# Optimization experiments

Hardware: AMD Instinct MI355X
Metric: run time of the kernel (lower is better)

Reference implementation:

```python
import jax, jax.numpy as jnp
import numpy as np

N1 = 50000; N2 = 50000; E1 = 800000; E2 = 800000; A = 10000
D_IN = 128; NHID = 128; D_OUT = 128; RATIO = 0.5
N_SUP = int(N1 * RATIO)  # 25000 super nodes
K_HOPS = 10  # GCN(in, nhid, k=10)
NEG_INF = jnp.float32(-1e30)


def _edge_norm(src, dst, w, n):
    # symmetric degree normalization of edge weights
    deg = jax.ops.segment_sum(w, dst, num_segments=n) + 1.0
    return w * jax.lax.rsqrt(deg[src] * deg[dst])


def _prop(h, src, dst, norm, n):
    # one round of weighted message passing: h'[v] = sum_e norm_e * h[src_e]
    return jax.ops.segment_sum(norm[:, None] * h[src], dst, num_segments=n)


def _gcn_k(x, src, dst, norm, n, W, b):
    h = x @ W + b
    for _ in range(K_HOPS):
        h = _prop(h, src, dst, norm, n)
    return h


def setup_inputs() -> dict:
    key = jax.random.key(0)
    ks = jax.random.split(key, 24)
    s = 0.05
    return {
        "x": jax.random.normal(ks[0], (N1, D_IN), jnp.float32),
        "edge_index": jax.random.randint(ks[1], (2, E1), 0, N1, jnp.int32),
        "edge_weight": jax.random.uniform(ks[2], (E1,), jnp.float32),
        "y": jax.random.normal(ks[3], (N2, D_IN), jnp.float32),
        "edge_index_y": jax.random.randint(ks[4], (2, E2), 0, N2, jnp.int32),
        "edge_weight_y": jax.random.uniform(ks[5], (E2,), jnp.float32),
        "anchor_links": jax.random.randint(ks[6], (2, A), 0, N1, jnp.int32),
        "temperature": 1,
        "W_gcn": jax.random.normal(ks[7], (D_IN, NHID), jnp.float32) * s,
        "b_gcn": jnp.zeros((NHID,), jnp.float32),
        "p_score": jax.random.normal(ks[8], (NHID,), jnp.float32) * s,
        "W_conv1": jax.random.normal(ks[9], (NHID, NHID), jnp.float32) * s,
        "b_conv1": jnp.zeros((NHID,), jnp.float32),
        "W_mlp1": jax.random.normal(ks[10], (NHID, NHID), jnp.float32) * s,
        "b_mlp1": jnp.zeros((NHID,), jnp.float32),
        "W_l1": jax.random.normal(ks[11], (NHID, NHID), jnp.float32) * s,
        "W_l2": jax.random.normal(ks[12], (NHID, NHID), jnp.float32) * s,
        "W_mlp2": jax.random.normal(ks[13], (NHID, D_OUT), jnp.float32) * s,
        "b_mlp2": jnp.zeros((D_OUT,), jnp.float32),
    }


def reference(x, edge_index, edge_weight, y, edge_index_y, edge_weight_y,
              anchor_links, temperature, W_gcn, b_gcn, p_score, W_conv1,
              b_conv1, W_mlp1, b_mlp1, W_l1, W_l2, W_mlp2, b_mlp2):
    T = jnp.float32(temperature)
    src, dst = edge_index[0], edge_index[1]
    norm1 = _edge_norm(src, dst, edge_weight, N1)

    # ---- down_convs[0]: 10-hop GCN on graph 1 ----
    out_x = _gcn_k(x, src, dst, norm1, N1, W_gcn, b_gcn)  # xs[0]
    xr = jax.nn.relu(out_x)

    # ---- TransPool: score -> top-k super nodes -> attention assignment ----
    s = xr @ p_score                             # [N1]
    _, perm = jax.lax.top_k(s, N_SUP)            # original ids of super nodes
    sup_id = jnp.full((N1,), -1, jnp.int32).at[perm].set(
        jnp.arange(N_SUP, dtype=jnp.int32))
    self_ids = jnp.arange(N1, dtype=src.dtype)
    cand_node = jnp.concatenate([src, self_ids])  # node being assigned
    cand_sup = jnp.concatenate([dst, self_ids])   # candidate super node
    valid = sup_id[cand_sup] >= 0
    att = jnp.sum(xr[cand_node] * xr[cand_sup], axis=-1)
    att = att / (jnp.sqrt(jnp.float32(NHID)) * T)
    att = jnp.where(valid, att, NEG_INF)
    m = jax.ops.segment_max(att, cand_node, num_segments=N1)
    e = jnp.exp(att - m[cand_node])
    esum = jax.ops.segment_sum(e, cand_node, num_segments=N1)
    w_soft = e / esum[cand_node]                 # per-node softmax over candidates
    is_best = valid & (att >= m[cand_node])
    cluster = jnp.full((N1,), -1, jnp.int32).at[cand_node].max(
        jnp.where(is_best, sup_id[cand_sup], -1))
    has = cluster >= 0
    cluster = jnp.maximum(cluster, 0)
    match = is_best & (sup_id[cand_sup] == cluster[cand_node])
    a = jnp.zeros((N1,), jnp.float32).at[cand_node].max(
        jnp.where(match, w_soft, 0.0))
    a = jnp.where(has, a, 0.0)                   # assign_weight (P1 values)

    # coarsen: x' = P x ; A' = P A P^T via cluster relabeling
    x_pool = jax.ops.segment_sum(a[:, None] * xr, cluster, num_segments=N_SUP)
    csrc, cdst = cluster[src], cluster[dst]
    cw = edge_weight * a[src] * a[dst]

    # ---- down_convs[1]: GCNConv on coarse graph (with self loop) ----
    norm_c = _edge_norm(csrc, cdst, cw, N_SUP)
    h2 = x_pool @ W_conv1 + b_conv1
    h2 = _prop(h2, csrc, cdst, norm_c, N_SUP) + h2
    sup1 = jax.nn.relu(h2)                       # xs[1]

    # ---- MLP1 ----
    sup2 = jax.nn.relu(sup1 @ W_mlp1 + b_mlp1)

    # ---- Q = P1 @ L (sparse-sparse matmul) ----
    a1, a2 = anchor_links[0], anchor_links[1]
    anchor_w = jnp.ones((A,), jnp.float32)
    q_sup = cluster[a1]
    q_col = a2
    q_w = a[a1] * anchor_w

    # ---- graph 2: shared down_convs[0] ----
    srcy, dsty = edge_index_y[0], edge_index_y[1]
    normy = _edge_norm(srcy, dsty, edge_weight_y, N2)
    out_y = _gcn_k(y, srcy, dsty, normy, N2, W_gcn, b_gcn)

    # ---- LastLayer: Q^T (sup2 W_l1) + L^T (out_x W_l2) scattered into graph2 ----
    t1 = sup2 @ W_l1
    out_y = out_y + jax.ops.segment_sum(q_w[:, None] * t1[q_sup], q_col,
                                        num_segments=N2)
    t2 = out_x @ W_l2
    out_y = out_y + jax.ops.segment_sum(anchor_w[:, None] * t2[a1], a2,
                                        num_segments=N2)

    recon_y = out_y @ W_mlp2 + b_mlp2
    return (out_x, sup1, out_y, sup2, a, recon_y)
```

## Files before the change

kernel.cpp:

```cpp
#include <hip/hip_runtime.h>
#include <hip/hip_bf16.h>
#include <math.h>

#define N1 50000
#define N2 50000
#define E1C 800000
#define E2C 800000
#define AC 10000
#define F 128
#define NSUP 25000
#define KHOPS 10
#define NEGINF -1e30f
#define NBINS 65536
#define NBINS22 (1 << 22)

static inline int cdiv(int a, int b) { return (a + b - 1) / b; }

__device__ __forceinline__ float bf2f(unsigned short u) {
  return __uint_as_float(((unsigned)u) << 16);
}
__device__ __forceinline__ unsigned short f2bf(float f) {
  unsigned x = __float_as_uint(f);
  return (unsigned short)((x + 0x7FFFu + ((x >> 16) & 1u)) >> 16);
}

__global__ void k_count(const int* __restrict__ key, int* __restrict__ cnt, int n) {
  int e = blockIdx.x * blockDim.x + threadIdx.x;
  if (e < n) atomicAdd(&cnt[key[e]], 1);
}

__global__ void k_scan(const int* __restrict__ cnt, int* __restrict__ rowptr, int n) {
  const int T = 1024;
  int t = threadIdx.x;
  int vpt = (n + T - 1) / T;
  int lo = t * vpt, hi = lo + vpt;
  if (hi > n) hi = n;
  int sum = 0;
  for (int i = lo; i < hi; ++i) sum += cnt[i];
  int lane = t & 63, wid = t >> 6;
  int v = sum;
#pragma unroll
  for (int o = 1; o < 64; o <<= 1) {
    int u = __shfl_up(v, o, 64);
    if (lane >= o) v += u;
  }
  __shared__ int wsum[16];
  if (lane == 63) wsum[wid] = v;
  __syncthreads();
  if (t < 16) {
    int w = wsum[t];
#pragma unroll
    for (int o = 1; o < 16; o <<= 1) {
      int u = __shfl_up(w, o, 64);
      if (t >= o) w += u;
    }
    wsum[t] = w;
  }
  __syncthreads();
  int base = (wid ? wsum[wid - 1] : 0) + (v - sum);
  if (t == 0) rowptr[0] = 0;
  int run = base;
  for (int i = lo; i < hi; ++i) { run += cnt[i]; rowptr[i + 1] = run; }
}

__global__ void k_fill(const int* __restrict__ key, const int* __restrict__ payload,
                       const float* __restrict__ val, const int* __restrict__ rowptr,
                       int* __restrict__ cnt, int* __restrict__ col, float* __restrict__ v,
                       int n) {
  int e = blockIdx.x * blockDim.x + threadIdx.x;
  if (e < n) {
    int k = key[e];
    int p = atomicAdd(&cnt[k], 1);
    int s = rowptr[k] + p;
    col[s] = payload[e];
    if (val) v[s] = val[e];
  }
}

__global__ void k_fill_iota(const int* __restrict__ key, const int* __restrict__ rowptr,
                            int* __restrict__ cnt, int* __restrict__ col, int n) {
  int e = blockIdx.x * blockDim.x + threadIdx.x;
  if (e < n) {
    int k = key[e];
    int p = atomicAdd(&cnt[k], 1);
    col[rowptr[k] + p] = e;
  }
}

__global__ void k_count_coarse(const int* __restrict__ dst, const int* __restrict__ cluster,
                               int* __restrict__ cnt, int n) {
  int e = blockIdx.x * blockDim.x + threadIdx.x;
  if (e < n) atomicAdd(&cnt[cluster[dst[e]]], 1);
}

__global__ void k_fill_coarse(const int* __restrict__ src, const int* __restrict__ dst,
                              const int* __restrict__ cluster, const float* __restrict__ w,
                              const float* __restrict__ a, const int* __restrict__ rowptr,
                              int* __restrict__ cnt, int* __restrict__ col,
                              float* __restrict__ v, int n) {
  int e = blockIdx.x * blockDim.x + threadIdx.x;
  if (e < n) {
    int sd = dst[e];
    int k = cluster[sd];
    int p = atomicAdd(&cnt[k], 1);
    int s = rowptr[k] + p;
    int ss = src[e];
    col[s] = cluster[ss];
    v[s] = w[e] * a[ss] * a[sd];
  }
}

__global__ void k_rowsum(const int* __restrict__ rowptr, const float* __restrict__ v,
                         float* __restrict__ deg, int n) {
  int row = blockIdx.x * 8 + (threadIdx.x >> 5);
  if (row >= n) return;
  int q = threadIdx.x & 31;
  int s0 = rowptr[row], s1 = rowptr[row + 1];
  float s = 0.f;
  for (int k = s0 + q; k < s1; k += 32) s += v[k];
#pragma unroll
  for (int o = 16; o; o >>= 1) s += __shfl_xor(s, o, 64);
  if (q == 0) deg[row] = s;
}

__global__ void k_csrnorm(const int* __restrict__ rowptr, const int* __restrict__ col,
                          float* __restrict__ v, const float* __restrict__ deg, int n) {
  int row = blockIdx.x * 8 + (threadIdx.x >> 5);
  if (row >= n) return;
  int q = threadIdx.x & 31;
  int s0 = rowptr[row], s1 = rowptr[row + 1];
  float di = deg[row] + 1.f;
  for (int s = s0 + q; s < s1; s += 32) {
    float dc = deg[col[s]] + 1.f;
    v[s] = v[s] / sqrtf(dc * di);
  }
}

__global__ void k_prop(const float4* __restrict__ hin, float4* __restrict__ hout,
                       float4* __restrict__ relu_out, const int* __restrict__ rowptr,
                       const int* __restrict__ col, const float* __restrict__ val, int n) {
  int node = blockIdx.x * 8 + (threadIdx.x >> 5);
  if (node >= n) return;
  int q = threadIdx.x & 31;
  int s0 = rowptr[node], s1 = rowptr[node + 1];
  float4 acc = make_float4(0.f, 0.f, 0.f, 0.f);
  for (int s = s0; s < s1; s += 8) {
    int c[8]; float v[8];
#pragma unroll
    for (int j = 0; j < 8; ++j) {
      int ss = s + j;
      int sc = (ss < s1) ? ss : (s1 - 1);
      c[j] = col[sc];
      v[j] = (ss < s1) ? val[sc] : 0.f;
    }
    float4 h[8];
#pragma unroll
    for (int j = 0; j < 8; ++j) h[j] = hin[(size_t)c[j] * 32 + q];
#pragma unroll
    for (int j = 0; j < 8; ++j) {
      acc.x = fmaf(v[j], h[j].x, acc.x);
      acc.y = fmaf(v[j], h[j].y, acc.y);
      acc.z = fmaf(v[j], h[j].z, acc.z);
      acc.w = fmaf(v[j], h[j].w, acc.w);
    }
  }
  hout[(size_t)node * 32 + q] = acc;
  if (relu_out) {
    float4 r;
    r.x = fmaxf(acc.x, 0.f); r.y = fmaxf(acc.y, 0.f);
    r.z = fmaxf(acc.z, 0.f); r.w = fmaxf(acc.w, 0.f);
    relu_out[(size_t)node * 32 + q] = r;
  }
}

__global__ void k_prop_bf16(const ushort4* __restrict__ hin, ushort4* __restrict__ hout,
                            float4* __restrict__ fout, const int* __restrict__ rowptr,
                            const int* __restrict__ col, const float* __restrict__ val, int n) {
  int node = blockIdx.x * 8 + (threadIdx.x >> 5);
  if (node >= n) return;
  int q = threadIdx.x & 31;
  int s0 = rowptr[node], s1 = rowptr[node + 1];
  float4 acc = make_float4(0.f, 0.f, 0.f, 0.f);
  for (int s = s0; s < s1; s += 8) {
    int c[8]; float v[8];
#pragma unroll
    for (int j = 0; j < 8; ++j) {
      int ss = s + j;
      int sc = (ss < s1) ? ss : (s1 - 1);
      c[j] = col[sc];
      v[j] = (ss < s1) ? val[sc] : 0.f;
    }
    ushort4 h[8];
#pragma unroll
    for (int j = 0; j < 8; ++j) h[j] = hin[(size_t)c[j] * 32 + q];
#pragma unroll
    for (int j = 0; j < 8; ++j) {
      acc.x = fmaf(v[j], bf2f(h[j].x), acc.x);
      acc.y = fmaf(v[j], bf2f(h[j].y), acc.y);
      acc.z = fmaf(v[j], bf2f(h[j].z), acc.z);
      acc.w = fmaf(v[j], bf2f(h[j].w), acc.w);
    }
  }
  if (fout) {
    fout[(size_t)node * 32 + q] = acc;
  } else {
    ushort4 o;
    o.x = f2bf(acc.x); o.y = f2bf(acc.y); o.z = f2bf(acc.z); o.w = f2bf(acc.w);
    hout[(size_t)node * 32 + q] = o;
  }
}

__global__ void k_transpose(const float* __restrict__ W, float* __restrict__ WT) {
  int i = blockIdx.x * blockDim.x + threadIdx.x;
  if (i < F * F) { int k = i >> 7, c = i & 127; WT[c * F + k] = W[i]; }
}

__global__ void k_mm128(const float* __restrict__ X, const float* __restrict__ WT,
                        const float* __restrict__ bias, float* __restrict__ out,
                        int M, int relu) {
  __shared__ float4 xs[16][32];
  int tid = threadIdx.x;
  int c = tid & 127;
  int half = tid >> 7;
  int row0 = blockIdx.x * 16;
  for (int t = tid; t < 512; t += 256) {
    int r = t >> 5, k4 = t & 31;
    int gr = row0 + r;
    float4 v = make_float4(0.f, 0.f, 0.f, 0.f);
    if (gr < M) v = ((const float4*)X)[(size_t)gr * 32 + k4];
    xs[r][k4] = v;
  }
  __syncthreads();
  float acc[8];
#pragma unroll
  for (int r = 0; r < 8; ++r) acc[r] = 0.f;
  const float4* wrow = (const float4*)WT + (size_t)c * 32;
  for (int k4 = 0; k4 < 32; ++k4) {
    float4 w = wrow[k4];
#pragma unroll
    for (int r = 0; r < 8; ++r) {
      float4 xv = xs[half * 8 + r][k4];
      acc[r] = fmaf(xv.x, w.x, acc[r]);
      acc[r] = fmaf(xv.y, w.y, acc[r]);
      acc[r] = fmaf(xv.z, w.z, acc[r]);
      acc[r] = fmaf(xv.w, w.w, acc[r]);
    }
  }
  float bb = bias ? bias[c] : 0.f;
#pragma unroll
  for (int r = 0; r < 8; ++r) {
    int gr = row0 + half * 8 + r;
    if (gr < M) {
      float v = acc[r] + bb;
      if (relu) v = fmaxf(v, 0.f);
      out[(size_t)gr * F + c] = v;
    }
  }
}

__global__ void k_mm128_bf16(const float* __restrict__ X, const float* __restrict__ WT,
                             const float* __restrict__ bias, unsigned short* __restrict__ out,
                             int M) {
  __shared__ float4 xs[16][32];
  int tid = threadIdx.x;
  int c = tid & 127;
  int half = tid >> 7;
  int row0 = blockIdx.x * 16;
  for (int t = tid; t < 512; t += 256) {
    int r = t >> 5, k4 = t & 31;
    int gr = row0 + r;
    float4 v = make_float4(0.f, 0.f, 0.f, 0.f);
    if (gr < M) v = ((const float4*)X)[(size_t)gr * 32 + k4];
    xs[r][k4] = v;
  }
  __syncthreads();
  float acc[8];
#pragma unroll
  for (int r = 0; r < 8; ++r) acc[r] = 0.f;
  const float4* wrow = (const float4*)WT + (size_t)c * 32;
  for (int k4 = 0; k4 < 32; ++k4) {
    float4 w = wrow[k4];
#pragma unroll
    for (int r = 0; r < 8; ++r) {
      float4 xv = xs[half * 8 + r][k4];
      acc[r] = fmaf(xv.x, w.x, acc[r]);
      acc[r] = fmaf(xv.y, w.y, acc[r]);
      acc[r] = fmaf(xv.z, w.z, acc[r]);
      acc[r] = fmaf(xv.w, w.w, acc[r]);
    }
  }
  float bb = bias ? bias[c] : 0.f;
#pragma unroll
  for (int r = 0; r < 8; ++r) {
    int gr = row0 + half * 8 + r;
    if (gr < M) out[(size_t)gr * F + c] = f2bf(acc[r] + bb);
  }
}

__global__ void k_addrelu(const float* __restrict__ a, const float* __restrict__ b,
                          float* __restrict__ out, int n) {
  int i = blockIdx.x * blockDim.x + threadIdx.x;
  if (i < n) out[i] = fmaxf(a[i] + b[i], 0.f);
}

__global__ void k_score(const float* __restrict__ xr, const float* __restrict__ p,
                        float* __restrict__ s, int n) {
  int wid = (blockIdx.x * blockDim.x + threadIdx.x) >> 6;
  int lane = threadIdx.x & 63;
  if (wid >= n) return;
  const float* row = xr + (size_t)wid * F;
  float d = row[lane] * p[lane] + row[lane + 64] * p[lane + 64];
#pragma unroll
  for (int o = 32; o; o >>= 1) d += __shfl_xor(d, o, 64);
  if (lane == 0) s[wid] = d;
}

__device__ __forceinline__ unsigned sortkey(float f) {
  if (f == 0.f) f = 0.f;
  unsigned u = __float_as_uint(f);
  return (u & 0x80000000u) ? ~u : (u | 0x80000000u);
}

__global__ void k_key(const float* __restrict__ s, unsigned* __restrict__ key, int n) {
  int i = blockIdx.x * blockDim.x + threadIdx.x;
  if (i < n) key[i] = sortkey(s[i]);
}

__global__ void k_count_bins22(const unsigned* __restrict__ key, int* __restrict__ cnt, int n) {
  int i = blockIdx.x * blockDim.x + threadIdx.x;
  if (i < n) atomicAdd(&cnt[key[i] >> 10], 1);
}

__global__ void k_hist_blocksum(const int* __restrict__ cnt, int* __restrict__ partial) {
  int t = threadIdx.x;
  int base = blockIdx.x * 1024 + t * 4;
  int s = cnt[base] + cnt[base + 1] + cnt[base + 2] + cnt[base + 3];
#pragma unroll
  for (int o = 32; o; o >>= 1) s += __shfl_down(s, o, 64);
  __shared__ int ws[4];
  int lane = t & 63, w = t >> 6;
  if (lane == 0) ws[w] = s;
  __syncthreads();
  if (t == 0) partial[blockIdx.x] = ws[0] + ws[1] + ws[2] + ws[3];
}

__global__ void k_hist_apply(const int* __restrict__ cnt, const int* __restrict__ partialptr,
                             int* __restrict__ binptr) {
  int t = threadIdx.x;
  int base = blockIdx.x * 1024 + t * 4;
  int c0 = cnt[base], c1 = cnt[base + 1], c2 = cnt[base + 2], c3 = cnt[base + 3];
  int s = c0 + c1 + c2 + c3;
  int lane = t & 63, w = t >> 6;
  int v = s;
#pragma unroll
  for (int o = 1; o < 64; o <<= 1) {
    int u = __shfl_up(v, o, 64);
    if (lane >= o) v += u;
  }
  __shared__ int ws[4];
  if (lane == 63) ws[w] = v;
  __syncthreads();
  int wb = 0;
  for (int i = 0; i < w; ++i) wb += ws[i];
  int run = partialptr[blockIdx.x] + wb + (v - s);
  binptr[base + 1] = run + c0;
  binptr[base + 2] = run + c0 + c1;
  binptr[base + 3] = run + c0 + c1 + c2;
  binptr[base + 4] = run + s;
  if (blockIdx.x == 0 && t == 0) binptr[0] = 0;
}

__global__ void k_fill_bins22(const unsigned* __restrict__ key, const int* __restrict__ binptr,
                              int* __restrict__ cnt, int* __restrict__ bidx,
                              unsigned* __restrict__ bkey, int n) {
  int i = blockIdx.x * blockDim.x + threadIdx.x;
  if (i < n) {
    unsigned k = key[i];
    int b = k >> 10;
    int p = atomicAdd(&cnt[b], 1);
    int s = binptr[b] + p;
    bidx[s] = i;
    bkey[s] = k;
  }
}

__global__ void k_rank22(const unsigned* __restrict__ key, const int* __restrict__ binptr,
                         const int* __restrict__ bidx, const unsigned* __restrict__ bkey,
                         int* __restrict__ supid, int n) {
  int i = blockIdx.x * blockDim.x + threadIdx.x;
  if (i >= n) return;
  unsigned ki = key[i];
  int b = ki >> 10;
  int cnt = n - binptr[b + 1];
  int s1 = binptr[b + 1];
  for (int s = binptr[b]; s < s1; ++s) {
    unsigned kj = bkey[s];
    cnt += (kj > ki) || (kj == ki && bidx[s] < i);
  }
  supid[i] = (cnt < NSUP) ? cnt : -1;
}

__device__ __forceinline__ float read_T(const void* p) {
  int ib = *(const int*)p;
  float fb = __int_as_float(ib);
  if (ib >= 1 && ib < (1 << 20)) return (float)ib;
  if (fb > 1e-6f && fb < 1e6f) return fb;
  return 1.0f;
}

__global__ void k_att_a(const float* __restrict__ xr, const int* __restrict__ rowptr,
                        const int* __restrict__ col, const int* __restrict__ supid,
                        const void* __restrict__ tptr, float* __restrict__ att,
                        float* __restrict__ attself, float* __restrict__ mout, int n) {
  int wid = (blockIdx.x * blockDim.x + threadIdx.x) >> 6;
  int lane = threadIdx.x & 63;
  if (wid >= n) return;
  float inv = 1.0f / (sqrtf(128.0f) * read_T(tptr));
  const float* xn = xr + (size_t)wid * F;
  float x0 = xn[lane], x1 = xn[lane + 64];
  float d = x0 * x0 + x1 * x1;
#pragma unroll
  for (int o = 32; o; o >>= 1) d += __shfl_xor(d, o, 64);
  float av = (supid[wid] >= 0) ? d * inv : NEGINF;
  float m = av;
  if (lane == 0) attself[wid] = av;
  int s0 = rowptr[wid], s1 = rowptr[wid + 1];
  for (int s = s0; s < s1; s += 4) {
    int c[4]; bool ok[4];
#pragma unroll
    for (int j = 0; j < 4; ++j) {
      int ss = s + j;
      ok[j] = ss < s1;
      c[j] = col[ok[j] ? ss : (s1 - 1)];
    }
    float dd[4];
#pragma unroll
    for (int j = 0; j < 4; ++j) {
      const float* xc = xr + (size_t)c[j] * F;
      dd[j] = x0 * xc[lane] + x1 * xc[lane + 64];
    }
#pragma unroll
    for (int j = 0; j < 4; ++j) {
#pragma unroll
      for (int o = 32; o; o >>= 1) dd[j] += __shfl_xor(dd[j], o, 64);
    }
#pragma unroll
    for (int j = 0; j < 4; ++j) {
      if (ok[j]) {
        float a2 = (supid[c[j]] >= 0) ? dd[j] * inv : NEGINF;
        if (lane == 0) att[s + j] = a2;
        m = fmaxf(m, a2);
      }
    }
  }
  if (lane == 0) mout[wid] = m;
}

__global__ void k_att_b(const int* __restrict__ rowptr, const int* __restrict__ col,
                        const int* __restrict__ supid, const float* __restrict__ att,
                        const float* __restrict__ attself, const float* __restrict__ mv,
                        int* __restrict__ cluster, float* __restrict__ aout, int n) {
  int i = blockIdx.x * 8 + (threadIdx.x >> 5);
  if (i >= n) return;
  int q = threadIdx.x & 31;
  float m = mv[i];
  float as = attself[i];
  float esum = 0.f;
  int best = -1;
  if (q == 0) {
    esum = expf(as - m);
    if (as >= m) best = supid[i];
  }
  int s0 = rowptr[i], s1 = rowptr[i + 1];
  for (int s = s0 + q; s < s1; s += 32) {
    float av = att[s];
    esum += expf(av - m);
    if (av >= m) {
      int sid = supid[col[s]];
      if (sid > best) best = sid;
    }
  }
#pragma unroll
  for (int o = 16; o; o >>= 1) {
    esum += __shfl_xor(esum, o, 64);
    int ob = __shfl_xor(best, o, 64);
    if (ob > best) best = ob;
  }
  if (q == 0) {
    int has = best >= 0;
    cluster[i] = has ? best : 0;
    aout[i] = has ? 1.0f / esum : 0.0f;
  }
}

__global__ void k_xpool_pull(const float4* __restrict__ xr, const float* __restrict__ a,
                             const int* __restrict__ rowptrM, const int* __restrict__ memb,
                             float4* __restrict__ xpool, int n) {
  int c = blockIdx.x * 8 + (threadIdx.x >> 5);
  if (c >= n) return;
  int q = threadIdx.x & 31;
  int s0 = rowptrM[c], s1 = rowptrM[c + 1];
  float4 acc = make_float4(0.f, 0.f, 0.f, 0.f);
  for (int s = s0; s < s1; ++s) {
    int m = memb[s];
    float av = a[m];
    float4 h = xr[(size_t)m * 32 + q];
    acc.x = fmaf(av, h.x, acc.x);
    acc.y = fmaf(av, h.y, acc.y);
    acc.z = fmaf(av, h.z, acc.z);
    acc.w = fmaf(av, h.w, acc.w);
  }
  xpool[(size_t)c * 32 + q] = acc;
}

__global__ void k_scatter_q(const int* __restrict__ a1, const int* __restrict__ a2,
                            const int* __restrict__ cluster, const float* __restrict__ aarr,
                            const float* __restrict__ t1, float* __restrict__ outy, int nA) {
  int idx = blockIdx.x * blockDim.x + threadIdx.x;
  if (idx >= nA * F) return;
  int k = idx >> 7, f = idx & 127;
  int n1 = a1[k];
  float qw = aarr[n1];
  if (qw != 0.f)
    atomicAdd(&outy[(size_t)a2[k] * F + f], qw * t1[(size_t)cluster[n1] * F + f]);
}

__global__ void k_scatter_t2(const int* __restrict__ a1, const int* __restrict__ a2,
                             const float* __restrict__ t2, float* __restrict__ outy, int nA) {
  int idx = blockIdx.x * blockDim.x + threadIdx.x;
  if (idx >= nA * F) return;
  int k = idx >> 7, f = idx & 127;
  atomicAdd(&outy[(size_t)a2[k] * F + f], t2[(size_t)a1[k] * F + f]);
}

extern "C" void kernel_launch(void* const* d_in, const int* in_sizes, int n_in,
                              void* d_out, int out_size, void* d_ws, size_t ws_size,
                              hipStream_t stream) {
  (void)in_sizes; (void)n_in; (void)out_size; (void)ws_size;
  const float* x   = (const float*)d_in[0];
  const int*   ei  = (const int*)d_in[1];
  const float* w1  = (const float*)d_in[2];
  const float* y   = (const float*)d_in[3];
  const int*   eiy = (const int*)d_in[4];
  const float* wy  = (const float*)d_in[5];
  const int*   anc = (const int*)d_in[6];
  const void*  tmp = d_in[7];
  const float* W_gcn = (const float*)d_in[8];
  const float* b_gcn = (const float*)d_in[9];
  const float* p_sc  = (const float*)d_in[10];
  const float* W_c1  = (const float*)d_in[11];
  const float* b_c1  = (const float*)d_in[12];
  const float* W_m1  = (const float*)d_in[13];
  const float* b_m1  = (const float*)d_in[14];
  const float* W_l1  = (const float*)d_in[15];
  const float* W_l2  = (const float*)d_in[16];
  const float* W_m2  = (const float*)d_in[17];
  const float* b_m2  = (const float*)d_in[18];

  float* out   = (float*)d_out;
  float* out_x = out;
  float* sup1  = out_x + (size_t)N1 * F;
  float* out_y = sup1 + (size_t)NSUP * F;
  float* sup2  = out_y + (size_t)N2 * F;
  float* a_out = sup2 + (size_t)NSUP * F;
  float* recon = a_out + N1;

  char* wsb = (char*)d_ws;
  size_t off = 0;
  auto alloc = [&](size_t bytes) -> void* {
    void* p = wsb + off;
    off = (off + bytes + 255) & ~(size_t)255;
    return p;
  };
  float*    f_csr1v   = (float*)alloc((size_t)E1C * 4);
  int*      i_csr1c   = (int*)alloc((size_t)E1C * 4);
  int*      i_rowptr1 = (int*)alloc((size_t)(N1 + 1) * 4);
  float*    f_deg     = (float*)alloc((size_t)N1 * 4);
  int*      i_cnt     = (int*)alloc((size_t)(NBINS + 1) * 4);
  float*    f_ha      = (float*)alloc((size_t)N1 * F * 4);
  float*    f_hb      = (float*)alloc((size_t)N1 * F * 4);
  float*    f_xr      = (float*)alloc((size_t)N1 * F * 4);
  float*    f_s       = (float*)alloc((size_t)N1 * 4);
  unsigned* u_key     = (unsigned*)alloc((size_t)N1 * 4);
  int*      i_partial = (int*)alloc((size_t)4096 * 4);
  int*      i_partptr = (int*)alloc((size_t)4097 * 4);
  int*      i_bidx    = (int*)alloc((size_t)N1 * 4);
  unsigned* u_bkey    = (unsigned*)alloc((size_t)N1 * 4);
  int*      i_supid   = (int*)alloc((size_t)N1 * 4);
  int*      i_rowptrS = (int*)alloc((size_t)(N1 + 1) * 4);
  int*      i_csrSc   = (int*)alloc((size_t)E1C * 4);
  float*    f_att     = (float*)alloc((size_t)E1C * 4);
  float*    f_attself = (float*)alloc((size_t)N1 * 4);
  float*    f_m       = (float*)alloc((size_t)N1 * 4);
  int*      i_cluster = (int*)alloc((size_t)N1 * 4);
  float*    f_xpool   = (float*)alloc((size_t)NSUP * F * 4);
  float*    f_degc    = (float*)alloc((size_t)NSUP * 4);
  int*      i_rowptrC = (int*)alloc((size_t)(NSUP + 1) * 4);
  int*      i_csrCc   = (int*)alloc((size_t)E1C * 4);
  float*    f_csrCv   = (float*)alloc((size_t)E1C * 4);
  int*      i_rowptrM = (int*)alloc((size_t)(NSUP + 1) * 4);
  int*      i_memb    = (int*)alloc((size_t)N1 * 4);
  float*    f_h2      = (float*)alloc((size_t)NSUP * F * 4);
  float*    f_h2p     = (float*)alloc((size_t)NSUP * F * 4);
  float*    f_wt      = (float*)alloc((size_t)6 * F * F * 4);

  int* i_cnt22    = (int*)f_ha;
  int* i_binptr22 = (int*)f_hb;
  unsigned short* h16a = (unsigned short*)f_ha;
  unsigned short* h16b = (unsigned short*)f_hb;

  const int* src1 = ei,  * dst1 = ei + E1C;
  const int* srcy = eiy, * dsty = eiy + E2C;
  const int* a1 = anc, * a2 = anc + AC;

  const float* Ws[6] = { W_gcn, W_c1, W_m1, W_l1, W_l2, W_m2 };
  for (int i = 0; i < 6; ++i)
    k_transpose<<<cdiv(F * F, 256), 256, 0, stream>>>(Ws[i], f_wt + (size_t)i * F * F);
  float* wt_gcn = f_wt, *wt_c1 = f_wt + 16384, *wt_m1 = f_wt + 2 * 16384,
       * wt_l1 = f_wt + 3 * 16384, *wt_l2 = f_wt + 4 * 16384, *wt_m2 = f_wt + 5 * 16384;

  int gE = cdiv(E1C, 256);
  int gN = cdiv(N1, 256);
  int gN8 = cdiv(N1, 8);
  int gC8 = cdiv(NSUP, 8);

  hipMemsetAsync(i_cnt, 0, (size_t)(NBINS + 1) * 4, stream);
  k_count<<<gE, 256, 0, stream>>>(dst1, i_cnt, E1C);
  k_scan<<<1, 1024, 0, stream>>>(i_cnt, i_rowptr1, N1);
  hipMemsetAsync(i_cnt, 0, (size_t)(NBINS + 1) * 4, stream);
  k_fill<<<gE, 256, 0, stream>>>(dst1, src1, w1, i_rowptr1, i_cnt, i_csr1c, f_csr1v, E1C);
  k_rowsum<<<gN8, 256, 0, stream>>>(i_rowptr1, f_csr1v, f_deg, N1);
  k_csrnorm<<<gN8, 256, 0, stream>>>(i_rowptr1, i_csr1c, f_csr1v, f_deg, N1);

  k_mm128<<<cdiv(N1, 16), 256, 0, stream>>>(x, wt_gcn, b_gcn, f_ha, N1, 0);
  {
    const float* cur = f_ha;
    for (int i = 0; i < KHOPS; ++i) {
      int last = (i == KHOPS - 1);
      float* dst = last ? out_x : ((i & 1) ? f_ha : f_hb);
      k_prop<<<gN8, 256, 0, stream>>>((const float4*)cur, (float4*)dst,
                                      last ? (float4*)f_xr : nullptr,
                                      i_rowptr1, i_csr1c, f_csr1v, N1);
      cur = dst;
    }
  }

  k_score<<<cdiv(N1, 4), 256, 0, stream>>>(f_xr, p_sc, f_s, N1);
  k_key<<<gN, 256, 0, stream>>>(f_s, u_key, N1);
  hipMemsetAsync(i_cnt22, 0, (size_t)NBINS22 * 4, stream);
  k_count_bins22<<<gN, 256, 0, stream>>>(u_key, i_cnt22, N1);
  k_hist_blocksum<<<NBINS22 / 1024, 256, 0, stream>>>(i_cnt22, i_partial);
  k_scan<<<1, 1024, 0, stream>>>(i_partial, i_partptr, 4096);
  k_hist_apply<<<NBINS22 / 1024, 256, 0, stream>>>(i_cnt22, i_partptr, i_binptr22);
  hipMemsetAsync(i_cnt22, 0, (size_t)NBINS22 * 4, stream);
  k_fill_bins22<<<gN, 256, 0, stream>>>(u_key, i_binptr22, i_cnt22, i_bidx, u_bkey, N1);
  k_rank22<<<gN, 256, 0, stream>>>(u_key, i_binptr22, i_bidx, u_bkey, i_supid, N1);

  hipMemsetAsync(i_cnt, 0, (size_t)(NBINS + 1) * 4, stream);
  k_count<<<gE, 256, 0, stream>>>(src1, i_cnt, E1C);
  k_scan<<<1, 1024, 0, stream>>>(i_cnt, i_rowptrS, N1);
  hipMemsetAsync(i_cnt, 0, (size_t)(NBINS + 1) * 4, stream);
  k_fill<<<gE, 256, 0, stream>>>(src1, dst1, (const float*)nullptr, i_rowptrS, i_cnt, i_csrSc,
                                 (float*)nullptr, E1C);

  k_att_a<<<cdiv(N1, 4), 256, 0, stream>>>(f_xr, i_rowptrS, i_csrSc, i_supid, tmp,
                                           f_att, f_attself, f_m, N1);
  k_att_b<<<gN8, 256, 0, stream>>>(i_rowptrS, i_csrSc, i_supid, f_att, f_attself,
                                   f_m, i_cluster, a_out, N1);

  hipMemsetAsync(i_cnt, 0, (size_t)(NBINS + 1) * 4, stream);
  k_count<<<gN, 256, 0, stream>>>(i_cluster, i_cnt, N1);
  k_scan<<<1, 1024, 0, stream>>>(i_cnt, i_rowptrM, NSUP);
  hipMemsetAsync(i_cnt, 0, (size_t)(NBINS + 1) * 4, stream);
  k_fill_iota<<<gN, 256, 0, stream>>>(i_cluster, i_rowptrM, i_cnt, i_memb, N1);
  k_xpool_pull<<<gC8, 256, 0, stream>>>((const float4*)f_xr, a_out, i_rowptrM,
                                        i_memb, (float4*)f_xpool, NSUP);

  hipMemsetAsync(i_cnt, 0, (size_t)(NBINS + 1) * 4, stream);
  k_count_coarse<<<gE, 256, 0, stream>>>(dst1, i_cluster, i_cnt, E1C);
  k_scan<<<1, 1024, 0, stream>>>(i_cnt, i_rowptrC, NSUP);
  hipMemsetAsync(i_cnt, 0, (size_t)(NBINS + 1) * 4, stream);
  k_fill_coarse<<<gE, 256, 0, stream>>>(src1, dst1, i_cluster, w1, a_out, i_rowptrC, i_cnt,
                                        i_csrCc, f_csrCv, E1C);
  k_rowsum<<<gC8, 256, 0, stream>>>(i_rowptrC, f_csrCv, f_degc, NSUP);
  k_csrnorm<<<gC8, 256, 0, stream>>>(i_rowptrC, i_csrCc, f_csrCv, f_degc, NSUP);

  k_mm128<<<cdiv(NSUP, 16), 256, 0, stream>>>(f_xpool, wt_c1, b_c1, f_h2, NSUP, 0);
  k_prop<<<gC8, 256, 0, stream>>>((const float4*)f_h2, (float4*)f_h2p, nullptr,
                                  i_rowptrC, i_csrCc, f_csrCv, NSUP);
  k_addrelu<<<cdiv(NSUP * F, 256), 256, 0, stream>>>(f_h2p, f_h2, sup1, NSUP * F);
  k_mm128<<<cdiv(NSUP, 16), 256, 0, stream>>>(sup1, wt_m1, b_m1, sup2, NSUP, 1);

  hipMemsetAsync(i_cnt, 0, (size_t)(NBINS + 1) * 4, stream);
  k_count<<<gE, 256, 0, stream>>>(dsty, i_cnt, E2C);
  k_scan<<<1, 1024, 0, stream>>>(i_cnt, i_rowptr1, N2);
  hipMemsetAsync(i_cnt, 0, (size_t)(NBINS + 1) * 4, stream);
  k_fill<<<gE, 256, 0, stream>>>(dsty, srcy, wy, i_rowptr1, i_cnt, i_csr1c, f_csr1v, E2C);
  k_rowsum<<<gN8, 256, 0, stream>>>(i_rowptr1, f_csr1v, f_deg, N2);
  k_csrnorm<<<gN8, 256, 0, stream>>>(i_rowptr1, i_csr1c, f_csr1v, f_deg, N2);
  k_mm128_bf16<<<cdiv(N2, 16), 256, 0, stream>>>(y, wt_gcn, b_gcn, h16a, N2);
  {
    const unsigned short* cur = h16a;
    for (int i = 0; i < KHOPS; ++i) {
      int last = (i == KHOPS - 1);
      unsigned short* dst = (i & 1) ? h16a : h16b;
      k_prop_bf16<<<gN8, 256, 0, stream>>>(
          (const ushort4*)cur, last ? nullptr : (ushort4*)dst,
          last ? (float4*)out_y : nullptr, i_rowptr1, i_csr1c, f_csr1v, N2);
      cur = dst;
    }
  }

  float* f_t1 = f_h2p;
  float* f_t2 = f_xr;
  k_mm128<<<cdiv(NSUP, 16), 256, 0, stream>>>(sup2, wt_l1, (const float*)nullptr, f_t1, NSUP, 0);
  k_scatter_q<<<cdiv(AC * F, 256), 256, 0, stream>>>(a1, a2, i_cluster, a_out, f_t1, out_y, AC);
  k_mm128<<<cdiv(N1, 16), 256, 0, stream>>>(out_x, wt_l2, (const float*)nullptr, f_t2, N1, 0);
  k_scatter_t2<<<cdiv(AC * F, 256), 256, 0, stream>>>(a1, a2, f_t2, out_y, AC);

  k_mm128<<<cdiv(N2, 16), 256, 0, stream>>>(out_y, wt_m2, b_m2, recon, N2, 0);
}
```

Baseline: 2.418 ms.

## Chunk feature layout per XCD so each propagation pass gathers from an L2-resident slice

The GCN hop features are stored in column-chunked layout: 8 chunks of 16 fp32 features for graph 1, and 4 chunks of 32 bf16 features for graph 2. Block indices are mapped so each XCD (blockIdx & 7) handles one chunk, so the random neighbor gathers of each hop hit a feature slice small enough to stay in that XCD's L2. Edge index and weight loads and intermediate stores use nontemporal hints to avoid polluting cache. The cost is that every CSR row walk is repeated once per chunk, and the block-to-XCD mapping it relies on is a hardware scheduling assumption.

```diff
diff --git a/kernel.cpp b/kernel.cpp
--- a/kernel.cpp
+++ b/kernel.cpp
@@ -15,6 +15,9 @@
 #define NBINS22 (1 << 22)
 
 static inline int cdiv(int a, int b) { return (a + b - 1) / b; }
+
+typedef float v4f __attribute__((ext_vector_type(4)));
+typedef unsigned int v4u __attribute__((ext_vector_type(4)));
 
 __device__ __forceinline__ float bf2f(unsigned short u) {
   return __uint_as_float(((unsigned)u) << 16);
@@ -173,40 +176,110 @@
   }
 }
 
-__global__ void k_prop_bf16(const ushort4* __restrict__ hin, ushort4* __restrict__ hout,
-                            float4* __restrict__ fout, const int* __restrict__ rowptr,
-                            const int* __restrict__ col, const float* __restrict__ val, int n) {
-  int node = blockIdx.x * 8 + (threadIdx.x >> 5);
+__global__ void k_prop_c(const float* __restrict__ hin, float* __restrict__ hout,
+                         float4* __restrict__ outx_std, float4* __restrict__ xr_std,
+                         const int* __restrict__ rowptr, const int* __restrict__ col,
+                         const float* __restrict__ val, int n) {
+  int chunk = blockIdx.x & 7;
+  int node = (blockIdx.x >> 3) * 64 + (threadIdx.x >> 2);
   if (node >= n) return;
-  int q = threadIdx.x & 31;
+  int sub = threadIdx.x & 3;
+  const float4* hc = (const float4*)hin + (size_t)chunk * n * 4;
   int s0 = rowptr[node], s1 = rowptr[node + 1];
   float4 acc = make_float4(0.f, 0.f, 0.f, 0.f);
-  for (int s = s0; s < s1; s += 8) {
-    int c[8]; float v[8];
-#pragma unroll
-    for (int j = 0; j < 8; ++j) {
+  for (int s = s0; s < s1; s += 4) {
+    int c[4]; float v[4];
+#pragma unroll
+    for (int j = 0; j < 4; ++j) {
       int ss = s + j;
       int sc = (ss < s1) ? ss : (s1 - 1);
-      c[j] = col[sc];
-      v[j] = (ss < s1) ? val[sc] : 0.f;
-    }
-    ushort4 h[8];
-#pragma unroll
-    for (int j = 0; j < 8; ++j) h[j] = hin[(size_t)c[j] * 32 + q];
-#pragma unroll
-    for (int j = 0; j < 8; ++j) {
-      acc.x = fmaf(v[j], bf2f(h[j].x), acc.x);
-      acc.y = fmaf(v[j], bf2f(h[j].y), acc.y);
-      acc.z = fmaf(v[j], bf2f(h[j].z), acc.z);
-      acc.w = fmaf(v[j], bf2f(h[j].w), acc.w);
-    }
-  }
-  if (fout) {
-    fout[(size_t)node * 32 + q] = acc;
+      c[j] = __builtin_nontemporal_load(col + sc);
+      float vv = __builtin_nontemporal_load(val + sc);
+      v[j] = (ss < s1) ? vv : 0.f;
+    }
+    float4 h[4];
+#pragma unroll
+    for (int j = 0; j < 4; ++j) h[j] = hc[(size_t)c[j] * 4 + sub];
+#pragma unroll
+    for (int j = 0; j < 4; ++j) {
+      acc.x = fmaf(v[j], h[j].x, acc.x);
+      acc.y = fmaf(v[j], h[j].y, acc.y);
+      acc.z = fmaf(v[j], h[j].z, acc.z);
+      acc.w = fmaf(v[j], h[j].w, acc.w);
+    }
+  }
+  if (outx_std) {
+    size_t o = (size_t)node * 32 + chunk * 4 + sub;
+    outx_std[o] = acc;
+    float4 r;
+    r.x = fmaxf(acc.x, 0.f); r.y = fmaxf(acc.y, 0.f);
+    r.z = fmaxf(acc.z, 0.f); r.w = fmaxf(acc.w, 0.f);
+    xr_std[o] = r;
   } else {
-    ushort4 o;
-    o.x = f2bf(acc.x); o.y = f2bf(acc.y); o.z = f2bf(acc.z); o.w = f2bf(acc.w);
-    hout[(size_t)node * 32 + q] = o;
+    v4f av = { acc.x, acc.y, acc.z, acc.w };
+    __builtin_nontemporal_store(av,
+        (v4f*)hout + ((size_t)chunk * n + node) * 4 + sub);
+  }
+}
+
+__global__ void k_prop_cb(const unsigned short* __restrict__ hin,
+                          unsigned short* __restrict__ hout,
+                          float4* __restrict__ outy_std,
+                          const int* __restrict__ rowptr, const int* __restrict__ col,
+                          const float* __restrict__ val, int n) {
+  int xcd = blockIdx.x & 7;
+  int chunk = xcd >> 1;
+  int nb = (blockIdx.x >> 3) * 2 + (xcd & 1);
+  int node = nb * 64 + (threadIdx.x >> 2);
+  if (node >= n) return;
+  int sub = threadIdx.x & 3;
+  const uint4* hc = (const uint4*)hin + (size_t)chunk * n * 4;
+  int s0 = rowptr[node], s1 = rowptr[node + 1];
+  float acc[8];
+#pragma unroll
+  for (int i = 0; i < 8; ++i) acc[i] = 0.f;
+  for (int s = s0; s < s1; s += 4) {
+    int c[4]; float v[4];
+#pragma unroll
+    for (int j = 0; j < 4; ++j) {
+      int ss = s + j;
+      int sc = (ss < s1) ? ss : (s1 - 1);
+      c[j] = __builtin_nontemporal_load(col + sc);
+      float vv = __builtin_nontemporal_load(val + sc);
+      v[j] = (ss < s1) ? vv : 0.f;
+    }
+    uint4 h[4];
+#pragma unroll
+    for (int j = 0; j < 4; ++j) h[j] = hc[(size_t)c[j] * 4 + sub];
+#pragma unroll
+    for (int j = 0; j < 4; ++j) {
+      unsigned u;
+      u = h[j].x;
+      acc[0] = fmaf(v[j], bf2f((unsigned short)u), acc[0]);
+      acc[1] = fmaf(v[j], bf2f((unsigned short)(u >> 16)), acc[1]);
+      u = h[j].y;
+      acc[2] = fmaf(v[j], bf2f((unsigned short)u), acc[2]);
+      acc[3] = fmaf(v[j], bf2f((unsigned short)(u >> 16)), acc[3]);
+      u = h[j].z;
+      acc[4] = fmaf(v[j], bf2f((unsigned short)u), acc[4]);
+      acc[5] = fmaf(v[j], bf2f((unsigned short)(u >> 16)), acc[5]);
+      u = h[j].w;
+      acc[6] = fmaf(v[j], bf2f((unsigned short)u), acc[6]);
+      acc[7] = fmaf(v[j], bf2f((unsigned short)(u >> 16)), acc[7]);
+    }
+  }
+  if (outy_std) {
+    size_t o = (size_t)node * 32 + chunk * 8 + sub * 2;
+    outy_std[o] = make_float4(acc[0], acc[1], acc[2], acc[3]);
+    outy_std[o + 1] = make_float4(acc[4], acc[5], acc[6], acc[7]);
+  } else {
+    v4u p;
+    p.x = (unsigned)f2bf(acc[0]) | ((unsigned)f2bf(acc[1]) << 16);
+    p.y = (unsigned)f2bf(acc[2]) | ((unsigned)f2bf(acc[3]) << 16);
+    p.z = (unsigned)f2bf(acc[4]) | ((unsigned)f2bf(acc[5]) << 16);
+    p.w = (unsigned)f2bf(acc[6]) | ((unsigned)f2bf(acc[7]) << 16);
+    __builtin_nontemporal_store(p,
+        (v4u*)hout + ((size_t)chunk * n + node) * 4 + sub);
   }
 }
 
@@ -217,7 +290,7 @@
 
 __global__ void k_mm128(const float* __restrict__ X, const float* __restrict__ WT,
                         const float* __restrict__ bias, float* __restrict__ out,
-                        int M, int relu) {
+                        int M, int relu, int chunked) {
   __shared__ float4 xs[16][32];
   int tid = threadIdx.x;
   int c = tid & 127;
@@ -253,7 +326,10 @@
     if (gr < M) {
       float v = acc[r] + bb;
       if (relu) v = fmaxf(v, 0.f);
-      out[(size_t)gr * F + c] = v;
+      if (chunked)
+        out[((size_t)(c >> 4) * M + gr) * 16 + (c & 15)] = v;
+      else
+        out[(size_t)gr * F + c] = v;
     }
   }
 }
@@ -293,7 +369,8 @@
 #pragma unroll
   for (int r = 0; r < 8; ++r) {
     int gr = row0 + half * 8 + r;
-    if (gr < M) out[(size_t)gr * F + c] = f2bf(acc[r] + bb);
+    if (gr < M)
+      out[((size_t)(c >> 5) * M + gr) * 32 + (c & 31)] = f2bf(acc[r] + bb);
   }
 }
 
@@ -623,6 +700,8 @@
   int gN = cdiv(N1, 256);
   int gN8 = cdiv(N1, 8);
   int gC8 = cdiv(NSUP, 8);
+  int gP1 = 8 * cdiv(N1, 64);
+  int gP2 = 8 * cdiv(cdiv(N2, 64), 2);
 
   hipMemsetAsync(i_cnt, 0, (size_t)(NBINS + 1) * 4, stream);
   k_count<<<gE, 256, 0, stream>>>(dst1, i_cnt, E1C);
@@ -632,15 +711,16 @@
   k_rowsum<<<gN8, 256, 0, stream>>>(i_rowptr1, f_csr1v, f_deg, N1);
   k_csrnorm<<<gN8, 256, 0, stream>>>(i_rowptr1, i_csr1c, f_csr1v, f_deg, N1);
 
-  k_mm128<<<cdiv(N1, 16), 256, 0, stream>>>(x, wt_gcn, b_gcn, f_ha, N1, 0);
+  k_mm128<<<cdiv(N1, 16), 256, 0, stream>>>(x, wt_gcn, b_gcn, f_ha, N1, 0, 1);
   {
     const float* cur = f_ha;
     for (int i = 0; i < KHOPS; ++i) {
       int last = (i == KHOPS - 1);
-      float* dst = last ? out_x : ((i & 1) ? f_ha : f_hb);
-      k_prop<<<gN8, 256, 0, stream>>>((const float4*)cur, (float4*)dst,
-                                      last ? (float4*)f_xr : nullptr,
-                                      i_rowptr1, i_csr1c, f_csr1v, N1);
+      float* dst = (i & 1) ? f_ha : f_hb;
+      k_prop_c<<<gP1, 256, 0, stream>>>(cur, dst,
+                                        last ? (float4*)out_x : nullptr,
+                                        last ? (float4*)f_xr : nullptr,
+                                        i_rowptr1, i_csr1c, f_csr1v, N1);
       cur = dst;
     }
   }
@@ -685,11 +765,11 @@
   k_rowsum<<<gC8, 256, 0, stream>>>(i_rowptrC, f_csrCv, f_degc, NSUP);
   k_csrnorm<<<gC8, 256, 0, stream>>>(i_rowptrC, i_csrCc, f_csrCv, f_degc, NSUP);
 
-  k_mm128<<<cdiv(NSUP, 16), 256, 0, stream>>>(f_xpool, wt_c1, b_c1, f_h2, NSUP, 0);
+  k_mm128<<<cdiv(NSUP, 16), 256, 0, stream>>>(f_xpool, wt_c1, b_c1, f_h2, NSUP, 0, 0);
   k_prop<<<gC8, 256, 0, stream>>>((const float4*)f_h2, (float4*)f_h2p, nullptr,
                                   i_rowptrC, i_csrCc, f_csrCv, NSUP);
   k_addrelu<<<cdiv(NSUP * F, 256), 256, 0, stream>>>(f_h2p, f_h2, sup1, NSUP * F);
-  k_mm128<<<cdiv(NSUP, 16), 256, 0, stream>>>(sup1, wt_m1, b_m1, sup2, NSUP, 1);
+  k_mm128<<<cdiv(NSUP, 16), 256, 0, stream>>>(sup1, wt_m1, b_m1, sup2, NSUP, 1, 0);
 
   hipMemsetAsync(i_cnt, 0, (size_t)(NBINS + 1) * 4, stream);
   k_count<<<gE, 256, 0, stream>>>(dsty, i_cnt, E2C);
@@ -704,19 +784,19 @@
     for (int i = 0; i < KHOPS; ++i) {
       int last = (i == KHOPS - 1);
       unsigned short* dst = (i & 1) ? h16a : h16b;
-      k_prop_bf16<<<gN8, 256, 0, stream>>>(
-          (const ushort4*)cur, last ? nullptr : (ushort4*)dst,
-          last ? (float4*)out_y : nullptr, i_rowptr1, i_csr1c, f_csr1v, N2);
+      k_prop_cb<<<gP2, 256, 0, stream>>>(cur, dst,
+                                         last ? (float4*)out_y : nullptr,
+                                         i_rowptr1, i_csr1c, f_csr1v, N2);
       cur = dst;
     }
   }
 
   float* f_t1 = f_h2p;
   float* f_t2 = f_xr;
-  k_mm128<<<cdiv(NSUP, 16), 256, 0, stream>>>(sup2, wt_l1, (const float*)nullptr, f_t1, NSUP, 0);
+  k_mm128<<<cdiv(NSUP, 16), 256, 0, stream>>>(sup2, wt_l1, (const float*)nullptr, f_t1, NSUP, 0, 0);
   k_scatter_q<<<cdiv(AC * F, 256), 256, 0, stream>>>(a1, a2, i_cluster, a_out, f_t1, out_y, AC);
-  k_mm128<<<cdiv(N1, 16), 256, 0, stream>>>(out_x, wt_l2, (const float*)nullptr, f_t2, N1, 0);
+  k_mm128<<<cdiv(N1, 16), 256, 0, stream>>>(out_x, wt_l2, (const float*)nullptr, f_t2, N1, 0, 0);
   k_scatter_t2<<<cdiv(AC * F, 256), 256, 0, stream>>>(a1, a2, f_t2, out_y, AC);
 
-  k_mm128<<<cdiv(N2, 16), 256, 0, stream>>>(out_y, wt_m2, b_m2, recon, N2, 0);
-}
+  k_mm128<<<cdiv(N2, 16), 256, 0, stream>>>(out_y, wt_m2, b_m2, recon, N2, 0, 0);
+}
```

Result: slower. 3.527 ms (+45.9%).

## Split graph-1 propagation features into XCC-local 16-column chunks with work stealing

Applied to the files above, without the earlier changes.

The graph-1 feature matrix is stored as eight 16-column chunks, each contiguous across nodes, and a new propagation kernel processes one chunk per block. Blocks take work from per-XCC atomic counters (read via s_getreg) so that each chunk's gathers tend to stay within one XCC's L2, aiming to raise cache hit rates for the random neighbor gathers. CSR reads and intermediate stores use nontemporal hints. In exchange, the CSR index and value arrays are re-read once per chunk, and the design depends on the hardware register id mapping and on counters reset once per call.

```diff
diff --git a/kernel.cpp b/kernel.cpp
--- a/kernel.cpp
+++ b/kernel.cpp
@@ -16,12 +16,20 @@
 
 static inline int cdiv(int a, int b) { return (a + b - 1) / b; }
 
+typedef float v2f __attribute__((ext_vector_type(2)));
+
 __device__ __forceinline__ float bf2f(unsigned short u) {
   return __uint_as_float(((unsigned)u) << 16);
 }
 __device__ __forceinline__ unsigned short f2bf(float f) {
   unsigned x = __float_as_uint(f);
   return (unsigned short)((x + 0x7FFFu + ((x >> 16) & 1u)) >> 16);
+}
+
+__device__ __forceinline__ int xcc_id() {
+  int v;
+  asm volatile("s_getreg_b32 %0, hwreg(20, 0, 32)" : "=s"(v));
+  return v;
 }
 
 __global__ void k_count(const int* __restrict__ key, int* __restrict__ cnt, int n) {
@@ -173,6 +181,63 @@
   }
 }
 
+__global__ void k_prop_c16(const float* __restrict__ hin, float* __restrict__ hout,
+                           float* __restrict__ outx_std, float* __restrict__ xr_std,
+                           const int* __restrict__ rowptr, const int* __restrict__ col,
+                           const float* __restrict__ val, int* __restrict__ wctr, int n) {
+  const int M = (N1 + 31) >> 5;
+  __shared__ int s_item;
+  if (threadIdx.x == 0) {
+    int xcc = xcc_id();
+    int item = -1;
+    for (int t = 0; t < 8; ++t) {
+      int c = (xcc + t) & 7;
+      int i = atomicAdd(&wctr[c], 1);
+      if (i < M) { item = c * M + i; break; }
+    }
+    s_item = item;
+  }
+  __syncthreads();
+  int item = s_item;
+  if (item < 0) return;
+  int chunk = item / M;
+  int node = (item % M) * 32 + (threadIdx.x >> 3);
+  if (node >= n) return;
+  int sub = threadIdx.x & 7;
+  const float2* hc = (const float2*)hin + (size_t)chunk * n * 8;
+  int s0 = rowptr[node], s1 = rowptr[node + 1];
+  float2 acc = make_float2(0.f, 0.f);
+  for (int s = s0; s < s1; s += 8) {
+    int c[8]; float v[8];
+#pragma unroll
+    for (int j = 0; j < 8; ++j) {
+      int ss = s + j;
+      int sc = (ss < s1) ? ss : (s1 - 1);
+      c[j] = __builtin_nontemporal_load(col + sc);
+      float vv = __builtin_nontemporal_load(val + sc);
+      v[j] = (ss < s1) ? vv : 0.f;
+    }
+    float2 h[8];
+#pragma unroll
+    for (int j = 0; j < 8; ++j) h[j] = hc[(size_t)c[j] * 8 + sub];
+#pragma unroll
+    for (int j = 0; j < 8; ++j) {
+      acc.x = fmaf(v[j], h[j].x, acc.x);
+      acc.y = fmaf(v[j], h[j].y, acc.y);
+    }
+  }
+  if (outx_std) {
+    size_t o = (size_t)node * 64 + chunk * 8 + sub;
+    ((float2*)outx_std)[o] = acc;
+    float2 r = make_float2(fmaxf(acc.x, 0.f), fmaxf(acc.y, 0.f));
+    ((float2*)xr_std)[o] = r;
+  } else {
+    v2f a2 = { acc.x, acc.y };
+    __builtin_nontemporal_store(a2,
+        (v2f*)hout + (size_t)chunk * n * 8 + (size_t)node * 8 + sub);
+  }
+}
+
 __global__ void k_prop_bf16(const ushort4* __restrict__ hin, ushort4* __restrict__ hout,
                             float4* __restrict__ fout, const int* __restrict__ rowptr,
                             const int* __restrict__ col, const float* __restrict__ val, int n) {
@@ -217,7 +282,7 @@
 
 __global__ void k_mm128(const float* __restrict__ X, const float* __restrict__ WT,
                         const float* __restrict__ bias, float* __restrict__ out,
-                        int M, int relu) {
+                        int M, int relu, int chunked) {
   __shared__ float4 xs[16][32];
   int tid = threadIdx.x;
   int c = tid & 127;
@@ -253,7 +318,10 @@
     if (gr < M) {
       float v = acc[r] + bb;
       if (relu) v = fmaxf(v, 0.f);
-      out[(size_t)gr * F + c] = v;
+      if (chunked)
+        out[((size_t)(c >> 4) * M + gr) * 16 + (c & 15)] = v;
+      else
+        out[(size_t)gr * F + c] = v;
     }
   }
 }
@@ -603,6 +671,7 @@
   float*    f_h2      = (float*)alloc((size_t)NSUP * F * 4);
   float*    f_h2p     = (float*)alloc((size_t)NSUP * F * 4);
   float*    f_wt      = (float*)alloc((size_t)6 * F * F * 4);
+  int*      i_wctr    = (int*)alloc((size_t)16 * 8 * 4);
 
   int* i_cnt22    = (int*)f_ha;
   int* i_binptr22 = (int*)f_hb;
@@ -613,6 +682,7 @@
   const int* srcy = eiy, * dsty = eiy + E2C;
   const int* a1 = anc, * a2 = anc + AC;
 
+  hipMemsetAsync(i_wctr, 0, (size_t)16 * 8 * 4, stream);
   const float* Ws[6] = { W_gcn, W_c1, W_m1, W_l1, W_l2, W_m2 };
   for (int i = 0; i < 6; ++i)
     k_transpose<<<cdiv(F * F, 256), 256, 0, stream>>>(Ws[i], f_wt + (size_t)i * F * F);
@@ -623,6 +693,7 @@
   int gN = cdiv(N1, 256);
   int gN8 = cdiv(N1, 8);
   int gC8 = cdiv(NSUP, 8);
+  int gP1 = 8 * cdiv(N1, 32);
 
   hipMemsetAsync(i_cnt, 0, (size_t)(NBINS + 1) * 4, stream);
   k_count<<<gE, 256, 0, stream>>>(dst1, i_cnt, E1C);
@@ -632,15 +703,17 @@
   k_rowsum<<<gN8, 256, 0, stream>>>(i_rowptr1, f_csr1v, f_deg, N1);
   k_csrnorm<<<gN8, 256, 0, stream>>>(i_rowptr1, i_csr1c, f_csr1v, f_deg, N1);
 
-  k_mm128<<<cdiv(N1, 16), 256, 0, stream>>>(x, wt_gcn, b_gcn, f_ha, N1, 0);
+  k_mm128<<<cdiv(N1, 16), 256, 0, stream>>>(x, wt_gcn, b_gcn, f_ha, N1, 0, 1);
   {
     const float* cur = f_ha;
     for (int i = 0; i < KHOPS; ++i) {
       int last = (i == KHOPS - 1);
-      float* dst = last ? out_x : ((i & 1) ? f_ha : f_hb);
-      k_prop<<<gN8, 256, 0, stream>>>((const float4*)cur, (float4*)dst,
-                                      last ? (float4*)f_xr : nullptr,
-                                      i_rowptr1, i_csr1c, f_csr1v, N1);
+      float* dst = (i & 1) ? f_ha : f_hb;
+      k_prop_c16<<<gP1, 256, 0, stream>>>(cur, dst,
+                                          last ? out_x : nullptr,
+                                          last ? f_xr : nullptr,
+                                          i_rowptr1, i_csr1c, f_csr1v,
+                                          i_wctr + i * 8, N1);
       cur = dst;
     }
   }
@@ -685,11 +758,11 @@
   k_rowsum<<<gC8, 256, 0, stream>>>(i_rowptrC, f_csrCv, f_degc, NSUP);
   k_csrnorm<<<gC8, 256, 0, stream>>>(i_rowptrC, i_csrCc, f_csrCv, f_degc, NSUP);
 
-  k_mm128<<<cdiv(NSUP, 16), 256, 0, stream>>>(f_xpool, wt_c1, b_c1, f_h2, NSUP, 0);
+  k_mm128<<<cdiv(NSUP, 16), 256, 0, stream>>>(f_xpool, wt_c1, b_c1, f_h2, NSUP, 0, 0);
   k_prop<<<gC8, 256, 0, stream>>>((const float4*)f_h2, (float4*)f_h2p, nullptr,
                                   i_rowptrC, i_csrCc, f_csrCv, NSUP);
   k_addrelu<<<cdiv(NSUP * F, 256), 256, 0, stream>>>(f_h2p, f_h2, sup1, NSUP * F);
-  k_mm128<<<cdiv(NSUP, 16), 256, 0, stream>>>(sup1, wt_m1, b_m1, sup2, NSUP, 1);
+  k_mm128<<<cdiv(NSUP, 16), 256, 0, stream>>>(sup1, wt_m1, b_m1, sup2, NSUP, 1, 0);
 
   hipMemsetAsync(i_cnt, 0, (size_t)(NBINS + 1) * 4, stream);
   k_count<<<gE, 256, 0, stream>>>(dsty, i_cnt, E2C);
@@ -713,10 +786,10 @@
 
   float* f_t1 = f_h2p;
   float* f_t2 = f_xr;
-  k_mm128<<<cdiv(NSUP, 16), 256, 0, stream>>>(sup2, wt_l1, (const float*)nullptr, f_t1, NSUP, 0);
+  k_mm128<<<cdiv(NSUP, 16), 256, 0, stream>>>(sup2, wt_l1, (const float*)nullptr, f_t1, NSUP, 0, 0);
   k_scatter_q<<<cdiv(AC * F, 256), 256, 0, stream>>>(a1, a2, i_cluster, a_out, f_t1, out_y, AC);
-  k_mm128<<<cdiv(N1, 16), 256, 0, stream>>>(out_x, wt_l2, (const float*)nullptr, f_t2, N1, 0);
+  k_mm128<<<cdiv(N1, 16), 256, 0, stream>>>(out_x, wt_l2, (const float*)nullptr, f_t2, N1, 0, 0);
   k_scatter_t2<<<cdiv(AC * F, 256), 256, 0, stream>>>(a1, a2, f_t2, out_y, AC);
 
-  k_mm128<<<cdiv(N2, 16), 256, 0, stream>>>(out_y, wt_m2, b_m2, recon, N2, 0);
-}
+  k_mm128<<<cdiv(N2, 16), 256, 0, stream>>>(out_y, wt_m2, b_m2, recon, N2, 0, 0);
+}
```

Result: slower. 3.592 ms (+48.5%).
